# Optimization experiments

Measured on AMD Instinct MI355X. Metric: run time of the kernel, lower is better.

## Reference

```python
import jax, jax.numpy as jnp
import numpy as np

N = 50000      # num nodes
E = 800000     # num edges
F = 64         # in_channels
H = 4          # heads
C = 64         # out_channels
NEG_SLOPE = 0.2
SCALE = float(np.sqrt(F))  # scaled_product=True -> divide by sqrt(in_channels)


def setup_inputs() -> dict:
    key = jax.random.key(0)
    k1, k2, k3, k4, k5, k6 = jax.random.split(key, 6)
    x = jax.random.normal(k1, (N, F), dtype=jnp.float32)
    edge_index = jax.random.randint(k2, (2, E), 0, N, dtype=jnp.int32)
    edge_weight = jax.random.uniform(k3, (E, 1), dtype=jnp.float32)
    # learned parameters (glorot-ish scale)
    W_lin = jax.random.normal(k4, (F, H * C), dtype=jnp.float32) / np.sqrt(F)
    W_att = jax.random.normal(k5, (F, H * F), dtype=jnp.float32) / np.sqrt(F)
    bias = jnp.zeros((H * C,), dtype=jnp.float32)
    return {"x": x, "edge_index": edge_index, "edge_weight": edge_weight,
            "W_lin": W_lin, "W_att": W_att, "bias": bias}


def reference(x, edge_index, edge_weight, W_lin, W_att, bias):
    src = edge_index[0]  # j: source / message sender
    dst = edge_index[1]  # i: target / aggregation index

    # node transforms
    xs = (x @ W_lin).reshape(N, H, C)   # lin(x): values for messages
    u = (x @ W_att).reshape(N, H, F)    # lin_att(x): multiplicative attention keys

    # multiplicative attention score: x_j^T W_h x_i  -> [E, H]
    score = jnp.einsum('ehf,ef->eh', u[src], x[dst]) / SCALE
    score = jax.nn.leaky_relu(score, NEG_SLOPE)

    # masked scatter-softmax over incoming edges of each destination node
    smax = jax.ops.segment_max(jax.lax.stop_gradient(score), dst, num_segments=N)  # [N, H]
    e = jnp.exp(score - smax[dst]) * edge_weight                                   # mask = edge_weight
    denom = jax.ops.segment_sum(e, dst, num_segments=N) + 1e-16                    # [N, H]
    alpha = e / denom[dst]                                                         # [E, H]

    # message = alpha * x_src, aggregate (add) at destination
    out = jax.ops.segment_sum(alpha[:, :, None] * xs[src], dst, num_segments=N)    # [N, H, C]
    out = out.reshape(N, H * C) + bias                                             # concat heads + bias
    return out
```

## Files before the change

### kernel.cpp

```cpp
#include <hip/hip_runtime.h>
#include <hip/hip_bf16.h>
#include <math.h>

#define N_NODES 50000
#define N_EDGES 800000
#define GEMM_ROWS 32
#define AGG_NODES 32
#define PAD_EDGES (N_EDGES + N_NODES * 15)
#define QGEMM_BLOCKS ((N_NODES + GEMM_ROWS - 1) / GEMM_ROWS)
#define BASE_BLOCKS ((N_NODES + 255) / 256)
#define SCALE_FOLD 0.18033688011112042f
#define XT_STRIDE 34

typedef __attribute__((ext_vector_type(8))) short bf16x8_t;
typedef __attribute__((ext_vector_type(4))) float f32x4_t;

static __device__ __forceinline__ ushort bfrn(float v) {
  __hip_bfloat16 b = __float2bfloat16(v);
  return __builtin_bit_cast(ushort, b);
}
static __device__ __forceinline__ bf16x8_t as_bf16x8(uint4 u) {
  union { uint4 a; bf16x8_t b; } c; c.a = u; return c.b;
}
static __device__ __forceinline__ float bflo(uint u) {
  return __uint_as_float(u << 16);
}
static __device__ __forceinline__ float bfhi(uint u) {
  return __uint_as_float(u & 0xFFFF0000u);
}

__global__ __launch_bounds__(256) void hist_kernel(
    const int* __restrict__ dst, int* __restrict__ deg, int* __restrict__ epos,
    const float* __restrict__ Watt, float* __restrict__ Wt) {
  int e = blockIdx.x * 256 + threadIdx.x;
  if (e < 16384) {
    int c = e & 63;
    int r = (e >> 6) & 63;
    int h = e >> 12;
    Wt[e] = Watt[c * 256 + h * 64 + r] * SCALE_FOLD;
  }
  if (e < N_EDGES) epos[e] = atomicAdd(&deg[dst[e]], 1);
}

__global__ __launch_bounds__(256) void qgemm_base_kernel(
    const float* __restrict__ x, const float* __restrict__ Wt,
    uint2* __restrict__ q_t2, ushort* __restrict__ xhi,
    const int* __restrict__ deg, int* __restrict__ cursor,
    int2* __restrict__ offs2, int2* __restrict__ csr2) {
  const int tid = threadIdx.x;
  if (blockIdx.x >= QGEMM_BLOCKS) {
    const int i = (blockIdx.x - QGEMM_BLOCKS) * 256 + tid;
    const int lane = tid & 63;
    const int d = (i < N_NODES) ? deg[i] : 0;
    const int nt = (d + 15) >> 4;
    const int pd = nt << 4;
    int incl = pd;
#pragma unroll
    for (int m = 1; m < 64; m <<= 1) {
      int u = __shfl_up(incl, m);
      if (lane >= m) incl += u;
    }
    int wbase = 0;
    if (lane == 63) wbase = atomicAdd(cursor, incl);
    wbase = __shfl(wbase, 63);
    const int base = wbase + incl - pd;
    if (i < N_NODES) {
      offs2[i] = make_int2(base, nt);
      for (int j = d; j < pd; ++j) csr2[base + j] = make_int2(0, 0);
    }
    return;
  }
  __shared__ float xlds[GEMM_ROWS * 64];
  const int blk = blockIdx.x;
#pragma unroll
  for (int p = 0; p < 8; ++p) {
    int idx = p * 256 + tid;
    int gidx = blk * (GEMM_ROWS * 64) + idx;
    xlds[idx] = (gidx < N_NODES * 64) ? x[gidx] : 0.f;
  }
  __syncthreads();
  {
    int row = tid >> 3;
    int c0 = (tid & 7) * 8;
    int grow = blk * GEMM_ROWS + row;
    if (grow < N_NODES) {
      uint hu[4];
#pragma unroll
      for (int d2 = 0; d2 < 4; ++d2) {
        float v0 = xlds[row * 64 + c0 + 2 * d2];
        float v1 = xlds[row * 64 + c0 + 2 * d2 + 1];
        hu[d2] = (uint)bfrn(v0) | ((uint)bfrn(v1) << 16);
      }
      *(uint4*)(xhi + (size_t)grow * 64 + c0) =
          make_uint4(hu[0], hu[1], hu[2], hu[3]);
    }
  }
  const int c4 = tid & 63;
  const int h = c4 >> 4;
  const int f4 = c4 & 15;
  const int rg = (tid >> 6) * 8;
  const float4* Wv = (const float4*)Wt;
  float4 acc[8] = {};
  for (int g = 0; g < 64; ++g) {
    float4 w4 = Wv[(size_t)h * 1024 + g * 16 + f4];
#pragma unroll
    for (int r = 0; r < 8; ++r) {
      float a = xlds[(rg + r) * 64 + g];
      acc[r].x += a * w4.x; acc[r].y += a * w4.y;
      acc[r].z += a * w4.z; acc[r].w += a * w4.w;
    }
  }
#pragma unroll
  for (int r = 0; r < 8; ++r) {
    int row = blk * GEMM_ROWS + rg + r;
    if (row < N_NODES) {
      uint2 pk;
      pk.x = (uint)bfrn(acc[r].x) | ((uint)bfrn(acc[r].y) << 16);
      pk.y = (uint)bfrn(acc[r].z) | ((uint)bfrn(acc[r].w) << 16);
      q_t2[(size_t)row * 64 + c4] = pk;
    }
  }
}

__global__ __launch_bounds__(256) void scatter_kernel(
    const int* __restrict__ src, const int* __restrict__ dst,
    const float* __restrict__ ew, const int2* __restrict__ offs2,
    const int* __restrict__ epos, int2* __restrict__ csr2) {
  int e = blockIdx.x * 256 + threadIdx.x;
  if (e >= N_EDGES) return;
  int idx = offs2[dst[e]].x + epos[e];
  csr2[idx] = make_int2(src[e], __float_as_int(ew[e]));
}

__global__ __launch_bounds__(256) void aggregate_kernel(
    const uint4* __restrict__ qt4, const uint4* __restrict__ xhi4,
    const int2* __restrict__ offs2, const int2* __restrict__ csr2,
    ushort* __restrict__ agg) {
  __shared__ __attribute__((aligned(16))) ushort xt16[4][16][XT_STRIDE * 2];
  __shared__ __attribute__((aligned(16))) ushort pt[4][4][16];
  const int wave = threadIdx.x >> 6;
  const int node = blockIdx.x * 4 + wave;
  const int lane = threadIdx.x & 63;
  const int l15 = lane & 15;
  const int lg = lane >> 4;
  const int hq = l15 & 3;

  const bf16x8_t Qa = as_bf16x8(qt4[(size_t)node * 32 + hq * 8 + lg]);
  const bf16x8_t Qb = as_bf16x8(qt4[(size_t)node * 32 + hq * 8 + 4 + lg]);
  const int2 o2 = offs2[node];
  const int s0 = o2.x;
  const int ntiles = o2.y;

  const bf16x8_t ONES =
      as_bf16x8(make_uint4(0x3F803F80u, 0x3F803F80u, 0x3F803F80u, 0x3F803F80u));
  f32x4_t acc0 = {0.f, 0.f, 0.f, 0.f};
  f32x4_t acc1 = {0.f, 0.f, 0.f, 0.f};
  f32x4_t acc2 = {0.f, 0.f, 0.f, 0.f};
  f32x4_t acc3 = {0.f, 0.f, 0.f, 0.f};
  f32x4_t accL = {0.f, 0.f, 0.f, 0.f};

  const int eb = (lg & 1) * 8;

  for (int t = 0; t < ntiles; ++t) {
    const int k0 = s0 + t * 16;
    const int2 e2 = csr2[k0 + l15];
    const int j = e2.x;
    const float w = __int_as_float(e2.y);
    const uint4 ah0 = xhi4[(size_t)j * 8 + lg];
    const uint4 ah1 = xhi4[(size_t)j * 8 + 4 + lg];
    {
      ushort* xr = &xt16[wave][l15][0];
      *(uint2*)(xr + 8 * lg) = make_uint2(ah0.x, ah0.y);
      *(uint2*)(xr + 8 * lg + 4) = make_uint2(ah0.z, ah0.w);
      *(uint2*)(xr + 32 + 8 * lg) = make_uint2(ah1.x, ah1.y);
      *(uint2*)(xr + 32 + 8 * lg + 4) = make_uint2(ah1.z, ah1.w);
    }
    f32x4_t S = {0.f, 0.f, 0.f, 0.f};
    S = __builtin_amdgcn_mfma_f32_16x16x32_bf16(Qa, as_bf16x8(ah0), S, 0, 0, 0);
    S = __builtin_amdgcn_mfma_f32_16x16x32_bf16(Qb, as_bf16x8(ah1), S, 0, 0, 0);
    float p0 = exp2f(fmaxf(S[0], 0.2f * S[0])) * w;
    float p1 = exp2f(fmaxf(S[1], 0.2f * S[1])) * w;
    float p2 = exp2f(fmaxf(S[2], 0.2f * S[2])) * w;
    float p3 = exp2f(fmaxf(S[3], 0.2f * S[3])) * w;
    if (lg == 0) {
      pt[wave][0][l15] = bfrn(p0);
      pt[wave][1][l15] = bfrn(p1);
      pt[wave][2][l15] = bfrn(p2);
      pt[wave][3][l15] = bfrn(p3);
    }
    uint4 pau = make_uint4(0u, 0u, 0u, 0u);
    if (lg < 2) pau = *(const uint4*)&pt[wave][hq][8 * lg];
    const bf16x8_t pa = as_bf16x8(pau);
#pragma unroll
    for (int b = 0; b < 4; ++b) {
      const int fc = 16 * b + l15;
      uint bw0 = (uint)xt16[wave][eb + 0][fc] |
                 ((uint)xt16[wave][eb + 1][fc] << 16);
      uint bw1 = (uint)xt16[wave][eb + 2][fc] |
                 ((uint)xt16[wave][eb + 3][fc] << 16);
      uint bw2 = (uint)xt16[wave][eb + 4][fc] |
                 ((uint)xt16[wave][eb + 5][fc] << 16);
      uint bw3 = (uint)xt16[wave][eb + 6][fc] |
                 ((uint)xt16[wave][eb + 7][fc] << 16);
      const bf16x8_t bx = as_bf16x8(make_uint4(bw0, bw1, bw2, bw3));
      if (b == 0)
        acc0 = __builtin_amdgcn_mfma_f32_16x16x32_bf16(pa, bx, acc0, 0, 0, 0);
      else if (b == 1)
        acc1 = __builtin_amdgcn_mfma_f32_16x16x32_bf16(pa, bx, acc1, 0, 0, 0);
      else if (b == 2)
        acc2 = __builtin_amdgcn_mfma_f32_16x16x32_bf16(pa, bx, acc2, 0, 0, 0);
      else
        acc3 = __builtin_amdgcn_mfma_f32_16x16x32_bf16(pa, bx, acc3, 0, 0, 0);
    }
    accL = __builtin_amdgcn_mfma_f32_16x16x32_bf16(pa, ONES, accL, 0, 0, 0);
  }

  const float lpv = (lg == 0) ? accL[0]
                  : (lg == 1) ? accL[1]
                  : (lg == 2) ? accL[2] : accL[3];
  const float inv = 1.f / (lpv + 1e-16f);
  const float v0 = ((lg == 0) ? acc0[0] : (lg == 1) ? acc0[1]
                   : (lg == 2) ? acc0[2] : acc0[3]) * inv;
  const float v1 = ((lg == 0) ? acc1[0] : (lg == 1) ? acc1[1]
                   : (lg == 2) ? acc1[2] : acc1[3]) * inv;
  const float v2 = ((lg == 0) ? acc2[0] : (lg == 1) ? acc2[1]
                   : (lg == 2) ? acc2[2] : acc2[3]) * inv;
  const float v3 = ((lg == 0) ? acc3[0] : (lg == 1) ? acc3[1]
                   : (lg == 2) ? acc3[2] : acc3[3]) * inv;
  ushort* ap = agg + (size_t)node * 256 + lg * 64 + l15;
  ap[0] = bfrn(v0);
  ap[16] = bfrn(v1);
  ap[32] = bfrn(v2);
  ap[48] = bfrn(v3);
}

__global__ __launch_bounds__(256) void out_gemm_kernel(
    const ushort* __restrict__ agg, const float* __restrict__ Wlin,
    const float* __restrict__ bias, float* __restrict__ out) {
  __shared__ float4 atile[AGG_NODES][4][17];
  const int tid = threadIdx.x;
  const int node0 = blockIdx.x * AGG_NODES;
  const uint2* av = (const uint2*)agg;
#pragma unroll
  for (int p = 0; p < 8; ++p) {
    int idx = p * 256 + tid;
    int row = idx >> 6;
    int cc = idx & 63;
    if (node0 + row < N_NODES) {
      uint2 u = av[(size_t)(node0 + row) * 64 + cc];
      float4 f;
      f.x = bflo(u.x); f.y = bfhi(u.x);
      f.z = bflo(u.y); f.w = bfhi(u.y);
      atile[row][cc >> 4][cc & 15] = f;
    }
  }
  __syncthreads();
  const int c4 = tid & 63;
  const int ns = tid >> 6;
  const int hh = c4 >> 4;
  const float4* Wv = (const float4*)Wlin;
  float4 acc[8] = {};
  for (int g4 = 0; g4 < 16; ++g4) {
    float4 w0 = Wv[(size_t)(g4 * 4 + 0) * 64 + c4];
    float4 w1 = Wv[(size_t)(g4 * 4 + 1) * 64 + c4];
    float4 w2 = Wv[(size_t)(g4 * 4 + 2) * 64 + c4];
    float4 w3 = Wv[(size_t)(g4 * 4 + 3) * 64 + c4];
#pragma unroll
    for (int n = 0; n < 8; ++n) {
      float4 a = atile[ns * 8 + n][hh][g4];
      acc[n].x += a.x * w0.x + a.y * w1.x + a.z * w2.x + a.w * w3.x;
      acc[n].y += a.x * w0.y + a.y * w1.y + a.z * w2.y + a.w * w3.y;
      acc[n].z += a.x * w0.z + a.y * w1.z + a.z * w2.z + a.w * w3.z;
      acc[n].w += a.x * w0.w + a.y * w1.w + a.z * w2.w + a.w * w3.w;
    }
  }
  float4 bv = ((const float4*)bias)[c4];
#pragma unroll
  for (int n = 0; n < 8; ++n) {
    int node = node0 + ns * 8 + n;
    if (node < N_NODES) {
      float4 o;
      o.x = acc[n].x + bv.x; o.y = acc[n].y + bv.y;
      o.z = acc[n].z + bv.z; o.w = acc[n].w + bv.w;
      ((float4*)out)[(size_t)node * 64 + c4] = o;
    }
  }
}

extern "C" void kernel_launch(void* const* d_in, const int* in_sizes, int n_in,
                              void* d_out, int out_size, void* d_ws,
                              size_t ws_size, hipStream_t stream) {
  (void)in_sizes; (void)n_in; (void)out_size; (void)ws_size;
  const float* x    = (const float*)d_in[0];
  const int*   ei   = (const int*)d_in[1];
  const float* ew   = (const float*)d_in[2];
  const float* Wlin = (const float*)d_in[3];
  const float* Watt = (const float*)d_in[4];
  const float* bias = (const float*)d_in[5];
  float* out = (float*)d_out;

  const int* srcv = ei;
  const int* dstv = ei + N_EDGES;

  char* ws = (char*)d_ws;
  size_t off = 0;
  auto alloc = [&](size_t bytes) {
    void* p = ws + off;
    off += (bytes + 255) & ~(size_t)255;
    return p;
  };
  ushort* q_t   = (ushort*)alloc((size_t)N_NODES * 256 * 2);
  ushort* agg   = (ushort*)alloc((size_t)N_NODES * 256 * 2);
  ushort* xhi   = (ushort*)alloc((size_t)N_NODES * 64 * 2);
  int2*   offs2 = (int2*)alloc((size_t)N_NODES * 8);
  int2*   csr2  = (int2*)alloc((size_t)PAD_EDGES * 8);
  char* aggc = (char*)agg;
  int*   deg    = (int*)aggc;
  int*   cursor = (int*)(aggc + N_NODES * 4);
  int*   epos   = (int*)(aggc + 256 * 1024);
  float* Wt     = (float*)(aggc + 4 * 1024 * 1024);

  hipMemsetAsync(deg, 0, (size_t)(N_NODES + 64) * 4, stream);

  hist_kernel<<<(N_EDGES + 255) / 256, 256, 0, stream>>>(dstv, deg, epos,
                                                         Watt, Wt);
  qgemm_base_kernel<<<QGEMM_BLOCKS + BASE_BLOCKS, 256, 0, stream>>>(
      x, Wt, (uint2*)q_t, xhi, deg, cursor, offs2, csr2);
  scatter_kernel<<<(N_EDGES + 255) / 256, 256, 0, stream>>>(
      srcv, dstv, ew, offs2, epos, csr2);
  aggregate_kernel<<<N_NODES / 4, 256, 0, stream>>>(
      (const uint4*)q_t, (const uint4*)xhi, offs2, csr2, agg);
  out_gemm_kernel<<<(N_NODES + AGG_NODES - 1) / AGG_NODES, 256, 0, stream>>>(
      agg, Wlin, bias, out);
}
```

Before: 171.1 us.

## Fuse edge aggregation and output projection into one kernel via shared memory

Merges the aggregate kernel and the output GEMM kernel. Each block now has its 4 waves aggregate 16 nodes, four nodes per wave, and keeps the normalized results in fp32 in LDS. The block then applies W_lin and the bias directly. This removes the bf16 agg buffer round-trip through global memory and one kernel launch, and it drops a bf16 rounding step. In exchange, the block count falls fourfold, each wave processes nodes serially so warps stall on degree imbalance, LDS use per block grows, and the scratch buffers move to dedicated allocations.

```diff
diff --git a/kernel.cpp b/kernel.cpp
--- a/kernel.cpp
+++ b/kernel.cpp
@@ -5,7 +5,6 @@
 #define N_NODES 50000
 #define N_EDGES 800000
 #define GEMM_ROWS 32
-#define AGG_NODES 32
 #define PAD_EDGES (N_EDGES + N_NODES * 15)
 #define QGEMM_BLOCKS ((N_NODES + GEMM_ROWS - 1) / GEMM_ROWS)
 #define BASE_BLOCKS ((N_NODES + 255) / 256)
@@ -132,142 +131,129 @@
   csr2[idx] = make_int2(src[e], __float_as_int(ew[e]));
 }
 
-__global__ __launch_bounds__(256) void aggregate_kernel(
+__global__ __launch_bounds__(256) void agg_out_kernel(
     const uint4* __restrict__ qt4, const uint4* __restrict__ xhi4,
     const int2* __restrict__ offs2, const int2* __restrict__ csr2,
-    ushort* __restrict__ agg) {
+    const float* __restrict__ Wlin, const float* __restrict__ bias,
+    float* __restrict__ out) {
   __shared__ __attribute__((aligned(16))) ushort xt16[4][16][XT_STRIDE * 2];
   __shared__ __attribute__((aligned(16))) ushort pt[4][4][16];
-  const int wave = threadIdx.x >> 6;
-  const int node = blockIdx.x * 4 + wave;
-  const int lane = threadIdx.x & 63;
+  __shared__ __attribute__((aligned(16))) float4 atile[16][4][17];
+  const int tid = threadIdx.x;
+  const int wave = tid >> 6;
+  const int lane = tid & 63;
   const int l15 = lane & 15;
   const int lg = lane >> 4;
   const int hq = l15 & 3;
-
-  const bf16x8_t Qa = as_bf16x8(qt4[(size_t)node * 32 + hq * 8 + lg]);
-  const bf16x8_t Qb = as_bf16x8(qt4[(size_t)node * 32 + hq * 8 + 4 + lg]);
-  const int2 o2 = offs2[node];
-  const int s0 = o2.x;
-  const int ntiles = o2.y;
+  const int node0 = blockIdx.x * 16;
 
   const bf16x8_t ONES =
       as_bf16x8(make_uint4(0x3F803F80u, 0x3F803F80u, 0x3F803F80u, 0x3F803F80u));
-  f32x4_t acc0 = {0.f, 0.f, 0.f, 0.f};
-  f32x4_t acc1 = {0.f, 0.f, 0.f, 0.f};
-  f32x4_t acc2 = {0.f, 0.f, 0.f, 0.f};
-  f32x4_t acc3 = {0.f, 0.f, 0.f, 0.f};
-  f32x4_t accL = {0.f, 0.f, 0.f, 0.f};
-
   const int eb = (lg & 1) * 8;
 
-  for (int t = 0; t < ntiles; ++t) {
-    const int k0 = s0 + t * 16;
-    const int2 e2 = csr2[k0 + l15];
-    const int j = e2.x;
-    const float w = __int_as_float(e2.y);
-    const uint4 ah0 = xhi4[(size_t)j * 8 + lg];
-    const uint4 ah1 = xhi4[(size_t)j * 8 + 4 + lg];
-    {
-      ushort* xr = &xt16[wave][l15][0];
-      *(uint2*)(xr + 8 * lg) = make_uint2(ah0.x, ah0.y);
-      *(uint2*)(xr + 8 * lg + 4) = make_uint2(ah0.z, ah0.w);
-      *(uint2*)(xr + 32 + 8 * lg) = make_uint2(ah1.x, ah1.y);
-      *(uint2*)(xr + 32 + 8 * lg + 4) = make_uint2(ah1.z, ah1.w);
-    }
-    f32x4_t S = {0.f, 0.f, 0.f, 0.f};
-    S = __builtin_amdgcn_mfma_f32_16x16x32_bf16(Qa, as_bf16x8(ah0), S, 0, 0, 0);
-    S = __builtin_amdgcn_mfma_f32_16x16x32_bf16(Qb, as_bf16x8(ah1), S, 0, 0, 0);
-    float p0 = exp2f(fmaxf(S[0], 0.2f * S[0])) * w;
-    float p1 = exp2f(fmaxf(S[1], 0.2f * S[1])) * w;
-    float p2 = exp2f(fmaxf(S[2], 0.2f * S[2])) * w;
-    float p3 = exp2f(fmaxf(S[3], 0.2f * S[3])) * w;
-    if (lg == 0) {
-      pt[wave][0][l15] = bfrn(p0);
-      pt[wave][1][l15] = bfrn(p1);
-      pt[wave][2][l15] = bfrn(p2);
-      pt[wave][3][l15] = bfrn(p3);
-    }
-    uint4 pau = make_uint4(0u, 0u, 0u, 0u);
-    if (lg < 2) pau = *(const uint4*)&pt[wave][hq][8 * lg];
-    const bf16x8_t pa = as_bf16x8(pau);
-#pragma unroll
-    for (int b = 0; b < 4; ++b) {
-      const int fc = 16 * b + l15;
-      uint bw0 = (uint)xt16[wave][eb + 0][fc] |
-                 ((uint)xt16[wave][eb + 1][fc] << 16);
-      uint bw1 = (uint)xt16[wave][eb + 2][fc] |
-                 ((uint)xt16[wave][eb + 3][fc] << 16);
-      uint bw2 = (uint)xt16[wave][eb + 4][fc] |
-                 ((uint)xt16[wave][eb + 5][fc] << 16);
-      uint bw3 = (uint)xt16[wave][eb + 6][fc] |
-                 ((uint)xt16[wave][eb + 7][fc] << 16);
-      const bf16x8_t bx = as_bf16x8(make_uint4(bw0, bw1, bw2, bw3));
-      if (b == 0)
-        acc0 = __builtin_amdgcn_mfma_f32_16x16x32_bf16(pa, bx, acc0, 0, 0, 0);
-      else if (b == 1)
-        acc1 = __builtin_amdgcn_mfma_f32_16x16x32_bf16(pa, bx, acc1, 0, 0, 0);
-      else if (b == 2)
-        acc2 = __builtin_amdgcn_mfma_f32_16x16x32_bf16(pa, bx, acc2, 0, 0, 0);
-      else
-        acc3 = __builtin_amdgcn_mfma_f32_16x16x32_bf16(pa, bx, acc3, 0, 0, 0);
-    }
-    accL = __builtin_amdgcn_mfma_f32_16x16x32_bf16(pa, ONES, accL, 0, 0, 0);
-  }
-
-  const float lpv = (lg == 0) ? accL[0]
-                  : (lg == 1) ? accL[1]
-                  : (lg == 2) ? accL[2] : accL[3];
-  const float inv = 1.f / (lpv + 1e-16f);
-  const float v0 = ((lg == 0) ? acc0[0] : (lg == 1) ? acc0[1]
-                   : (lg == 2) ? acc0[2] : acc0[3]) * inv;
-  const float v1 = ((lg == 0) ? acc1[0] : (lg == 1) ? acc1[1]
-                   : (lg == 2) ? acc1[2] : acc1[3]) * inv;
-  const float v2 = ((lg == 0) ? acc2[0] : (lg == 1) ? acc2[1]
-                   : (lg == 2) ? acc2[2] : acc2[3]) * inv;
-  const float v3 = ((lg == 0) ? acc3[0] : (lg == 1) ? acc3[1]
-                   : (lg == 2) ? acc3[2] : acc3[3]) * inv;
-  ushort* ap = agg + (size_t)node * 256 + lg * 64 + l15;
-  ap[0] = bfrn(v0);
-  ap[16] = bfrn(v1);
-  ap[32] = bfrn(v2);
-  ap[48] = bfrn(v3);
-}
-
-__global__ __launch_bounds__(256) void out_gemm_kernel(
-    const ushort* __restrict__ agg, const float* __restrict__ Wlin,
-    const float* __restrict__ bias, float* __restrict__ out) {
-  __shared__ float4 atile[AGG_NODES][4][17];
-  const int tid = threadIdx.x;
-  const int node0 = blockIdx.x * AGG_NODES;
-  const uint2* av = (const uint2*)agg;
-#pragma unroll
-  for (int p = 0; p < 8; ++p) {
-    int idx = p * 256 + tid;
-    int row = idx >> 6;
-    int cc = idx & 63;
-    if (node0 + row < N_NODES) {
-      uint2 u = av[(size_t)(node0 + row) * 64 + cc];
-      float4 f;
-      f.x = bflo(u.x); f.y = bfhi(u.x);
-      f.z = bflo(u.y); f.w = bfhi(u.y);
-      atile[row][cc >> 4][cc & 15] = f;
-    }
+  for (int sub = 0; sub < 4; ++sub) {
+    const int node = node0 + wave * 4 + sub;
+    const bf16x8_t Qa = as_bf16x8(qt4[(size_t)node * 32 + hq * 8 + lg]);
+    const bf16x8_t Qb = as_bf16x8(qt4[(size_t)node * 32 + hq * 8 + 4 + lg]);
+    const int2 o2 = offs2[node];
+    const int s0 = o2.x;
+    const int ntiles = o2.y;
+
+    f32x4_t acc0 = {0.f, 0.f, 0.f, 0.f};
+    f32x4_t acc1 = {0.f, 0.f, 0.f, 0.f};
+    f32x4_t acc2 = {0.f, 0.f, 0.f, 0.f};
+    f32x4_t acc3 = {0.f, 0.f, 0.f, 0.f};
+    f32x4_t accL = {0.f, 0.f, 0.f, 0.f};
+
+    for (int t = 0; t < ntiles; ++t) {
+      const int k0 = s0 + t * 16;
+      const int2 e2 = csr2[k0 + l15];
+      const int j = e2.x;
+      const float w = __int_as_float(e2.y);
+      const uint4 ah0 = xhi4[(size_t)j * 8 + lg];
+      const uint4 ah1 = xhi4[(size_t)j * 8 + 4 + lg];
+      {
+        ushort* xr = &xt16[wave][l15][0];
+        *(uint2*)(xr + 8 * lg) = make_uint2(ah0.x, ah0.y);
+        *(uint2*)(xr + 8 * lg + 4) = make_uint2(ah0.z, ah0.w);
+        *(uint2*)(xr + 32 + 8 * lg) = make_uint2(ah1.x, ah1.y);
+        *(uint2*)(xr + 32 + 8 * lg + 4) = make_uint2(ah1.z, ah1.w);
+      }
+      f32x4_t S = {0.f, 0.f, 0.f, 0.f};
+      S = __builtin_amdgcn_mfma_f32_16x16x32_bf16(Qa, as_bf16x8(ah0), S, 0, 0,
+                                                  0);
+      S = __builtin_amdgcn_mfma_f32_16x16x32_bf16(Qb, as_bf16x8(ah1), S, 0, 0,
+                                                  0);
+      float p0 = exp2f(fmaxf(S[0], 0.2f * S[0])) * w;
+      float p1 = exp2f(fmaxf(S[1], 0.2f * S[1])) * w;
+      float p2 = exp2f(fmaxf(S[2], 0.2f * S[2])) * w;
+      float p3 = exp2f(fmaxf(S[3], 0.2f * S[3])) * w;
+      if (lg == 0) {
+        pt[wave][0][l15] = bfrn(p0);
+        pt[wave][1][l15] = bfrn(p1);
+        pt[wave][2][l15] = bfrn(p2);
+        pt[wave][3][l15] = bfrn(p3);
+      }
+      uint4 pau = make_uint4(0u, 0u, 0u, 0u);
+      if (lg < 2) pau = *(const uint4*)&pt[wave][hq][8 * lg];
+      const bf16x8_t pa = as_bf16x8(pau);
+#pragma unroll
+      for (int b = 0; b < 4; ++b) {
+        const int fc = 16 * b + l15;
+        uint bw0 = (uint)xt16[wave][eb + 0][fc] |
+                   ((uint)xt16[wave][eb + 1][fc] << 16);
+        uint bw1 = (uint)xt16[wave][eb + 2][fc] |
+                   ((uint)xt16[wave][eb + 3][fc] << 16);
+        uint bw2 = (uint)xt16[wave][eb + 4][fc] |
+                   ((uint)xt16[wave][eb + 5][fc] << 16);
+        uint bw3 = (uint)xt16[wave][eb + 6][fc] |
+                   ((uint)xt16[wave][eb + 7][fc] << 16);
+        const bf16x8_t bx = as_bf16x8(make_uint4(bw0, bw1, bw2, bw3));
+        if (b == 0)
+          acc0 = __builtin_amdgcn_mfma_f32_16x16x32_bf16(pa, bx, acc0, 0, 0, 0);
+        else if (b == 1)
+          acc1 = __builtin_amdgcn_mfma_f32_16x16x32_bf16(pa, bx, acc1, 0, 0, 0);
+        else if (b == 2)
+          acc2 = __builtin_amdgcn_mfma_f32_16x16x32_bf16(pa, bx, acc2, 0, 0, 0);
+        else
+          acc3 = __builtin_amdgcn_mfma_f32_16x16x32_bf16(pa, bx, acc3, 0, 0, 0);
+      }
+      accL = __builtin_amdgcn_mfma_f32_16x16x32_bf16(pa, ONES, accL, 0, 0, 0);
+    }
+
+    const float lpv = (lg == 0) ? accL[0]
+                    : (lg == 1) ? accL[1]
+                    : (lg == 2) ? accL[2] : accL[3];
+    const float inv = 1.f / (lpv + 1e-16f);
+    const float v0 = ((lg == 0) ? acc0[0] : (lg == 1) ? acc0[1]
+                     : (lg == 2) ? acc0[2] : acc0[3]) * inv;
+    const float v1 = ((lg == 0) ? acc1[0] : (lg == 1) ? acc1[1]
+                     : (lg == 2) ? acc1[2] : acc1[3]) * inv;
+    const float v2 = ((lg == 0) ? acc2[0] : (lg == 1) ? acc2[1]
+                     : (lg == 2) ? acc2[2] : acc2[3]) * inv;
+    const float v3 = ((lg == 0) ? acc3[0] : (lg == 1) ? acc3[1]
+                     : (lg == 2) ? acc3[2] : acc3[3]) * inv;
+    float* at = (float*)&atile[wave * 4 + sub][lg][0];
+    at[l15] = v0;
+    at[16 + l15] = v1;
+    at[32 + l15] = v2;
+    at[48 + l15] = v3;
   }
   __syncthreads();
+
   const int c4 = tid & 63;
   const int ns = tid >> 6;
   const int hh = c4 >> 4;
   const float4* Wv = (const float4*)Wlin;
-  float4 acc[8] = {};
+  float4 acc[4] = {};
   for (int g4 = 0; g4 < 16; ++g4) {
     float4 w0 = Wv[(size_t)(g4 * 4 + 0) * 64 + c4];
     float4 w1 = Wv[(size_t)(g4 * 4 + 1) * 64 + c4];
     float4 w2 = Wv[(size_t)(g4 * 4 + 2) * 64 + c4];
     float4 w3 = Wv[(size_t)(g4 * 4 + 3) * 64 + c4];
 #pragma unroll
-    for (int n = 0; n < 8; ++n) {
-      float4 a = atile[ns * 8 + n][hh][g4];
+    for (int n = 0; n < 4; ++n) {
+      float4 a = atile[ns * 4 + n][hh][g4];
       acc[n].x += a.x * w0.x + a.y * w1.x + a.z * w2.x + a.w * w3.x;
       acc[n].y += a.x * w0.y + a.y * w1.y + a.z * w2.y + a.w * w3.y;
       acc[n].z += a.x * w0.z + a.y * w1.z + a.z * w2.z + a.w * w3.z;
@@ -276,14 +262,11 @@
   }
   float4 bv = ((const float4*)bias)[c4];
 #pragma unroll
-  for (int n = 0; n < 8; ++n) {
-    int node = node0 + ns * 8 + n;
-    if (node < N_NODES) {
-      float4 o;
-      o.x = acc[n].x + bv.x; o.y = acc[n].y + bv.y;
-      o.z = acc[n].z + bv.z; o.w = acc[n].w + bv.w;
-      ((float4*)out)[(size_t)node * 64 + c4] = o;
-    }
+  for (int n = 0; n < 4; ++n) {
+    float4 o;
+    o.x = acc[n].x + bv.x; o.y = acc[n].y + bv.y;
+    o.z = acc[n].z + bv.z; o.w = acc[n].w + bv.w;
+    ((float4*)out)[(size_t)(node0 + ns * 4 + n) * 64 + c4] = o;
   }
 }
 
@@ -309,18 +292,17 @@
     off += (bytes + 255) & ~(size_t)255;
     return p;
   };
-  ushort* q_t   = (ushort*)alloc((size_t)N_NODES * 256 * 2);
-  ushort* agg   = (ushort*)alloc((size_t)N_NODES * 256 * 2);
-  ushort* xhi   = (ushort*)alloc((size_t)N_NODES * 64 * 2);
-  int2*   offs2 = (int2*)alloc((size_t)N_NODES * 8);
-  int2*   csr2  = (int2*)alloc((size_t)PAD_EDGES * 8);
-  char* aggc = (char*)agg;
-  int*   deg    = (int*)aggc;
-  int*   cursor = (int*)(aggc + N_NODES * 4);
-  int*   epos   = (int*)(aggc + 256 * 1024);
-  float* Wt     = (float*)(aggc + 4 * 1024 * 1024);
-
-  hipMemsetAsync(deg, 0, (size_t)(N_NODES + 64) * 4, stream);
+  ushort* q_t    = (ushort*)alloc((size_t)N_NODES * 256 * 2);
+  ushort* xhi    = (ushort*)alloc((size_t)N_NODES * 64 * 2);
+  int2*   offs2  = (int2*)alloc((size_t)N_NODES * 8);
+  int2*   csr2   = (int2*)alloc((size_t)PAD_EDGES * 8);
+  int*    deg    = (int*)alloc((size_t)N_NODES * 4);
+  int*    cursor = (int*)alloc(256);
+  int*    epos   = (int*)alloc((size_t)N_EDGES * 4);
+  float*  Wt     = (float*)alloc((size_t)64 * 256 * 4);
+
+  hipMemsetAsync(deg, 0, (size_t)N_NODES * 4, stream);
+  hipMemsetAsync(cursor, 0, 256, stream);
 
   hist_kernel<<<(N_EDGES + 255) / 256, 256, 0, stream>>>(dstv, deg, epos,
                                                          Watt, Wt);
@@ -328,8 +310,6 @@
       x, Wt, (uint2*)q_t, xhi, deg, cursor, offs2, csr2);
   scatter_kernel<<<(N_EDGES + 255) / 256, 256, 0, stream>>>(
       srcv, dstv, ew, offs2, epos, csr2);
-  aggregate_kernel<<<N_NODES / 4, 256, 0, stream>>>(
-      (const uint4*)q_t, (const uint4*)xhi, offs2, csr2, agg);
-  out_gemm_kernel<<<(N_NODES + AGG_NODES - 1) / AGG_NODES, 256, 0, stream>>>(
-      agg, Wlin, bias, out);
-}
+  agg_out_kernel<<<N_NODES / 16, 256, 0, stream>>>(
+      (const uint4*)q_t, (const uint4*)xhi, offs2, csr2, Wlin, bias, out);
+}
```

After: 261.5 us. +52.8%, slower.
